# Kernel optimization log

Measured on AMD Instinct MI355X. Metric: run time of the kernel, lower is better.

The kernel has to match this reference:

```python
import jax, jax.numpy as jnp
import numpy as np

# ---- constants from vecpar / module globals ----
N_SAMPLE = 500000
HID = 64       # shared_layers = [64]
HEAD = 32      # q*_layers width
PERIOD = 30
KAPPA, Y_BAR, B, C = 0.2, 2.0, 1.0, 0.1
GAMMA, RHO, SIGMA, DT = 1.2, 0.03, 0.03, 0.005


def _glorot(key, shape):
    fan_in, fan_out = shape
    std = (2.0 / (fan_in + fan_out)) ** 0.5
    return std * jax.random.normal(key, shape, dtype=jnp.float32)


def setup_inputs() -> dict:
    key = jax.random.key(0)
    ks = jax.random.split(key, 8)
    Y = jax.random.uniform(ks[0], (N_SAMPLE, 2), minval=0.05, maxval=5.0, dtype=jnp.float32)
    z = lambda n: jnp.zeros((n,), dtype=jnp.float32)
    return {
        'Y': Y,
        'W0': _glorot(ks[1], (2, HID)),   'b0': z(HID),
        'Wh1': _glorot(ks[2], (HID, HEAD)), 'bh1': z(HEAD), 'Wo1': _glorot(ks[3], (HEAD, 1)), 'bo1': z(1),
        'Wh2': _glorot(ks[4], (HID, HEAD)), 'bh2': z(HEAD), 'Wo2': _glorot(ks[5], (HEAD, 1)), 'bo2': z(1),
        'Wh3': _glorot(ks[6], (HID, HEAD)), 'bh3': z(HEAD), 'Wo3': _glorot(ks[7], (HEAD, 1)), 'bo3': z(1),
    }


def _net(Y2, Y3, W0, b0, Wh1, bh1, Wo1, bo1, Wh2, bh2, Wo2, bo2, Wh3, bh3, Wo3, bo3):
    # shared trunk: concat -> Dense(64) -> tanh; heads: Dense(32)->tanh->Dense(1)->exp
    h = jnp.tanh(jnp.concatenate([Y2, Y3], axis=1) @ W0 + b0)
    q1 = jnp.exp(jnp.tanh(h @ Wh1 + bh1) @ Wo1 + bo1)
    q2 = jnp.exp(jnp.tanh(h @ Wh2 + bh2) @ Wo2 + bo2)
    q3 = jnp.exp(jnp.tanh(h @ Wh3 + bh3) @ Wo3 + bo3)
    return q1, q2, q3


def _forward(Y, W0, b0, Wh1, bh1, Wo1, bo1, Wh2, bh2, Wo2, bo2, Wh3, bh3, Wo3, bo3):
    params = (W0, b0, Wh1, bh1, Wo1, bo1, Wh2, bh2, Wo2, bo2, Wh3, bh3, Wo3, bo3)
    f = lambda y2, y3: _net(y2, y3, *params)

    def q_and_grads(y2, y3):
        # per-row scalar sensitivities via two jvp passes (equiv. to tape.gradient)
        ones = jnp.ones_like(y2); zeros = jnp.zeros_like(y2)
        (q1, q2, q3), (d12, d22, d32) = jax.jvp(f, (y2, y3), (ones, zeros))
        _, (d13, d23, d33) = jax.jvp(f, (y2, y3), (zeros, ones))
        s11 = d12 * SIGMA / q1; s21 = d22 * SIGMA / q2; s31 = d32 * SIGMA / q3
        s12 = d13 * SIGMA / q1; s22 = d23 * SIGMA / q2; s32 = d33 * SIGMA / q3
        return (q1, q2, q3), (s11, s21, s31, s12, s22, s32)

    n = Y.shape[0]
    Y2 = Y[:, :1]; Y3 = Y[:, 1:2]
    (q1, q2, q3), (s11, s21, s31, s12, s22, s32) = q_and_grads(Y2, Y3)

    # dZ already scaled by sqrt(dt)
    noise = jnp.sqrt(jnp.asarray(DT, Y.dtype)) * jax.random.normal(
        jax.random.key(42), (PERIOD, n, 1, 2), dtype=Y.dtype)

    def step(carry, dZ):
        q1, q2, q3, Y2, Y3, s11, s21, s31, s12, s22, s32, loss = carry
        dZ1 = dZ[..., 0]; dZ2 = dZ[..., 1]
        W = q1 + q2 + q3
        q1h = q1 / W; q2h = q2 / W; q3h = 1 - q1h - q2h
        c = B * q1 - C * q1 ** 2 + Y2 + Y3
        sc1 = B * q1 * s11 - 2 * C * q1 ** 2 * s11 + SIGMA
        sc2 = B * q1 * s12 - 2 * C * q1 ** 2 * s12 + SIGMA
        sW1 = q1 * s11 + q2 * s21 + q3 * s31
        sW2 = q1 * s12 + q2 * s22 + q3 * s32
        g = GAMMA / (GAMMA - 1)
        sJ1 = g * (sc1 / c - sW1 / W); sJ2 = g * (sc2 / c - sW2 / W)
        p1 = (GAMMA * q1h * (s11 ** 2 + s12 ** 2)
              + GAMMA * q2h * (s11 * s21 + s12 * s22)
              + GAMMA * q3h * (s11 * s31 + s12 * s32)
              - (1 - GAMMA) * (sJ1 * s11 + sJ2 * s12))
        p2 = (GAMMA * q1h * (s11 * s21 + s12 * s22)
              + GAMMA * q2h * (s21 ** 2 + s22 ** 2)
              + GAMMA * q3h * (s21 * s31 + s22 * s32)
              - (1 - GAMMA) * (sJ1 * s21 + sJ2 * s22))
        p3 = (GAMMA * q1h * (s11 * s31 + s12 * s32)
              + GAMMA * q2h * (s21 * s31 + s22 * s32)
              + GAMMA * q3h * (s31 ** 2 + s32 ** 2)
              - (1 - GAMMA) * (sJ1 * s31 + sJ2 * s32))
        muY2 = KAPPA * (Y_BAR - Y2); muY3 = KAPPA * (Y_BAR - Y3)
        r = (RHO
             + GAMMA * ((B * q1 - 2 * C * q1 ** 2) * (p1 - (B - C * q1))
                        - C * q1 ** 2 * (s11 ** 2 + s12 ** 2) + muY2 + muY3) / c
             - GAMMA * (GAMMA + 1) / 2 * (sc1 ** 2 + sc2 ** 2) / c ** 2)
        r = r / (1 - GAMMA * (B * q1 - 2 * C * q1 ** 2) / c)
        mu1 = r + p1 - (B - C * q1)
        mu2 = r + p2 - Y2 / q2
        mu3 = r + p3 - Y3 / q3
        q1n = q1 * (1 + mu1 * DT + s11 * dZ1 + s12 * dZ2)
        q2n = q2 * (1 + mu2 * DT + s21 * dZ1 + s22 * dZ2)
        q3n = q3 * (1 + mu3 * DT + s31 * dZ1 + s32 * dZ2)
        Y2n = Y2 + muY2 * DT + SIGMA * dZ1
        Y3n = Y3 + muY3 * DT + SIGMA * dZ2
        (q1t, q2t, q3t), (ns11, ns21, ns31, ns12, ns22, ns32) = q_and_grads(Y2n, Y3n)
        loss = loss + jnp.sum((q1n - q1t) ** 2 + (q2n - q2t) ** 2 + (q3n - q3t) ** 2) / (n * PERIOD)
        return (q1n, q2n, q3n, Y2n, Y3n, ns11, ns21, ns31, ns12, ns22, ns32, loss), None

    init = (q1, q2, q3, Y2, Y3, s11, s21, s31, s12, s22, s32, jnp.asarray(0.0, Y.dtype))
    carry, _ = jax.lax.scan(step, init, noise)
    return carry[-1]


def reference(Y, W0, b0, Wh1, bh1, Wo1, bo1, Wh2, bh2, Wo2, bo2, Wh3, bh3, Wo3, bo3):
    return _forward(Y, W0, b0, Wh1, bh1, Wo1, bo1, Wh2, bh2, Wo2, bo2, Wh3, bh3, Wo3, bo3)
```

## Files before the change

kernel.cpp:

```cpp
#include <hip/hip_runtime.h>
#include <hip/hip_bf16.h>
#include <stdint.h>

#define NB 256
#define PERIOD 30

typedef __bf16  bf16x8 __attribute__((ext_vector_type(8)));
typedef float   f32x4  __attribute__((ext_vector_type(4)));
typedef float   f32x2  __attribute__((ext_vector_type(2)));
typedef unsigned int uint4v __attribute__((ext_vector_type(4)));

__device__ __forceinline__ float frcp(float x){ return __builtin_amdgcn_rcpf(x); }

__device__ __forceinline__ float fast_tanh(float x){
  float e = __expf(2.0f*x);
  return fmaf(-2.0f, frcp(e + 1.0f), 1.0f);
}

__device__ __forceinline__ unsigned int f2bfbits(float x){
  union { __hip_bfloat16 b; unsigned short u; } v;
  v.b = __float2bfloat16(x);
  return (unsigned int)v.u;
}
__device__ __forceinline__ unsigned int pack2bf(float lo, float hi){
  return f2bfbits(lo) | (f2bfbits(hi) << 16);
}

__device__ __forceinline__ void threefry2x32_k42(uint32_t x0, uint32_t x1,
                                                 uint32_t& o0, uint32_t& o1){
  const uint32_t ks0 = 0u, ks1 = 42u, ks2 = 0u ^ 42u ^ 0x1BD11BDAu;
  x0 += ks0; x1 += ks1;
#define TFR(rot) { x0 += x1; x1 = (x1 << (rot)) | (x1 >> (32 - (rot))); x1 ^= x0; }
  TFR(13) TFR(15) TFR(26) TFR(6)
  x0 += ks1; x1 += ks2 + 1u;
  TFR(17) TFR(29) TFR(16) TFR(24)
  x0 += ks2; x1 += ks0 + 2u;
  TFR(13) TFR(15) TFR(26) TFR(6)
  x0 += ks0; x1 += ks1 + 3u;
  TFR(17) TFR(29) TFR(16) TFR(24)
  x0 += ks1; x1 += ks2 + 4u;
  TFR(13) TFR(15) TFR(26) TFR(6)
  x0 += ks2; x1 += ks0 + 5u;
#undef TFR
  o0 = x0; o1 = x1;
}

__device__ __forceinline__ float normal_from_bits(uint32_t bits){
  float f = __uint_as_float((bits >> 9) | 0x3f800000u) - 1.0f;
  const float lo = -0.99999994f;
  float u = fmaf(f, 2.0f, lo);
  u = fmaxf(u, lo);
  float w = -log1pf(-u*u);
  float p;
  if (w < 5.0f){
    float ww = w - 2.5f;
    p = 2.81022636e-08f;
    p = fmaf(p, ww, 3.43273939e-07f);
    p = fmaf(p, ww, -3.5233877e-06f);
    p = fmaf(p, ww, -4.39150654e-06f);
    p = fmaf(p, ww, 0.00021858087f);
    p = fmaf(p, ww, -0.00125372503f);
    p = fmaf(p, ww, -0.00417768164f);
    p = fmaf(p, ww, 0.246640727f);
    p = fmaf(p, ww, 1.50140941f);
  } else {
    float ww = sqrtf(w) - 3.0f;
    p = -0.000200214257f;
    p = fmaf(p, ww, 0.000100950558f);
    p = fmaf(p, ww, 0.00134934322f);
    p = fmaf(p, ww, -0.00367342844f);
    p = fmaf(p, ww, 0.00573950773f);
    p = fmaf(p, ww, -0.0076224613f);
    p = fmaf(p, ww, 0.00943887047f);
    p = fmaf(p, ww, 1.00167406f);
    p = fmaf(p, ww, 2.83297682f);
  }
  return 1.41421356f * (p * u);
}

__device__ __forceinline__ void stage_tile(char* buf, int st, int grp, int colL,
    const unsigned int* hp, const unsigned int* up){
  if (grp == st){
    const int rbase = colL * 128;
    const int sw = (colL & 7) << 4;
#pragma unroll
    for (int w = 0; w < 8; ++w){
      int off = rbase + ((w * 16) ^ sw);
      *(uint4v*)(buf + off)        = uint4v{hp[w*4], hp[w*4+1], hp[w*4+2], hp[w*4+3]};
      *(uint4v*)(buf + 2048 + off) = uint4v{up[w*4], up[w*4+1], up[w*4+2], up[w*4+3]};
    }
  }
}

__device__ __forceinline__ void net_eval(
    float y2, float y3,
    const float* __restrict__ W0, const float* __restrict__ b0,
    char* sAw,
    const char* __restrict__ sBb,
    const float* __restrict__ sBH,
    const float* __restrict__ sWO,
    int colL, int grp,
    const float* bo_v,
    float& q1o, float& q2o, float& q3o,
    float& s11, float& s21, float& s31,
    float& s12, float& s22, float& s32)
{
  unsigned int hp[32], up[32];
#pragma unroll
  for (int d = 0; d < 32; ++d){
    f32x2 w0a = *(const f32x2*)(W0 + 2*d);
    f32x2 w0b = *(const f32x2*)(W0 + 64 + 2*d);
    f32x2 b0v = *(const f32x2*)(b0 + 2*d);
    f32x2 pre = y2 * w0a + (y3 * w0b + b0v);
    float hA = fast_tanh(pre.x), hB = fast_tanh(pre.y);
    f32x2 h  = {hA, hB};
    f32x2 u  = 1.0f - h * h;
    hp[d] = pack2bf(hA, hB);
    up[d] = pack2bf(u.x, u.y);
  }

  float qraw[3] = {0,0,0}, Araw[3] = {0,0,0}, Braw[3] = {0,0,0};
  const int bsw = (colL & 7) << 4;

#pragma unroll 1
  for (int st = 0; st < 4; ++st){
    int zr = 0;
    asm volatile("" : "+v"(zr));

    stage_tile(sAw, st, grp, colL, hp, up);

    bf16x8 afh[2], afu[2];
#pragma unroll
    for (int kt = 0; kt < 2; ++kt){
      int off = colL*128 + ((kt*64 + grp*16) ^ bsw);
      afh[kt] = *(const bf16x8*)(sAw + off);
      afu[kt] = *(const bf16x8*)(sAw + 2048 + off);
    }

#pragma unroll
    for (int hd = 0; hd < 3; ++hd){
      float aq = 0.0f, aA = 0.0f, aB = 0.0f;
#pragma unroll
      for (int nt = 0; nt < 2; ++nt){
        bf16x8 bW[2], bA[2], bB[2];
#pragma unroll
        for (int kt = 0; kt < 2; ++kt){
          int rbase2 = (hd*96 + nt*16 + colL) * 128;
          int ko = ((kt*64 + grp*16) ^ bsw);
          bW[kt] = *(const bf16x8*)(sBb + rbase2 + ko);
          bA[kt] = *(const bf16x8*)(sBb + rbase2 + 4096 + ko);
          bB[kt] = *(const bf16x8*)(sBb + rbase2 + 8192 + ko);
        }
        f32x4 bh4 = *(const f32x4*)(sBH + hd*32 + nt*16 + grp*4 + zr);
        f32x4 wo4 = *(const f32x4*)(sWO + hd*32 + nt*16 + grp*4 + zr);
        f32x4 cAT = bh4;
        f32x4 cA2 = {0,0,0,0}, cA3 = {0,0,0,0};
#pragma unroll
        for (int kt = 0; kt < 2; ++kt){
          cAT = __builtin_amdgcn_mfma_f32_16x16x32_bf16(bW[kt], afh[kt], cAT, 0, 0, 0);
          cA2 = __builtin_amdgcn_mfma_f32_16x16x32_bf16(bA[kt], afu[kt], cA2, 0, 0, 0);
          cA3 = __builtin_amdgcn_mfma_f32_16x16x32_bf16(bB[kt], afu[kt], cA3, 0, 0, 0);
        }
        float t0 = fast_tanh(cAT[0]);
        float t1 = fast_tanh(cAT[1]);
        float t2 = fast_tanh(cAT[2]);
        float t3 = fast_tanh(cAT[3]);
        aq = fmaf(t0, wo4[0], aq);
        aq = fmaf(t1, wo4[1], aq);
        aq = fmaf(t2, wo4[2], aq);
        aq = fmaf(t3, wo4[3], aq);
        float dt0 = fmaf(-t0, t0, 1.0f);
        float dt1 = fmaf(-t1, t1, 1.0f);
        float dt2 = fmaf(-t2, t2, 1.0f);
        float dt3 = fmaf(-t3, t3, 1.0f);
        aA = fmaf(dt0, cA2[0], aA);
        aA = fmaf(dt1, cA2[1], aA);
        aA = fmaf(dt2, cA2[2], aA);
        aA = fmaf(dt3, cA2[3], aA);
        aB = fmaf(dt0, cA3[0], aB);
        aB = fmaf(dt1, cA3[1], aB);
        aB = fmaf(dt2, cA3[2], aB);
        aB = fmaf(dt3, cA3[3], aB);
      }
      aq += __shfl_xor(aq, 16, 64);  aq += __shfl_xor(aq, 32, 64);
      aA += __shfl_xor(aA, 16, 64);  aA += __shfl_xor(aA, 32, 64);
      aB += __shfl_xor(aB, 16, 64);  aB += __shfl_xor(aB, 32, 64);
      bool keep = (st == grp);
      qraw[hd] = keep ? aq : qraw[hd];
      Araw[hd] = keep ? aA : Araw[hd];
      Braw[hd] = keep ? aB : Braw[hd];
    }
  }

  q1o = __expf(qraw[0] + bo_v[0]);
  q2o = __expf(qraw[1] + bo_v[1]);
  q3o = __expf(qraw[2] + bo_v[2]);
  s11 = Araw[0]; s21 = Araw[1]; s31 = Araw[2];
  s12 = Braw[0]; s22 = Braw[1]; s32 = Braw[2];
}

__global__ __launch_bounds__(NB)
void sim_kernel(const float* __restrict__ Y,
  const float* __restrict__ W0,  const float* __restrict__ b0,
  const float* __restrict__ Wh1, const float* __restrict__ bh1,
  const float* __restrict__ Wo1, const float* __restrict__ bo1,
  const float* __restrict__ Wh2, const float* __restrict__ bh2,
  const float* __restrict__ Wo2, const float* __restrict__ bo2,
  const float* __restrict__ Wh3, const float* __restrict__ bh3,
  const float* __restrict__ Wo3, const float* __restrict__ bo3,
  float* __restrict__ out, int n)
{
  __shared__ __align__(16) char sB[288 * 128];
  __shared__ __align__(16) char sA[4][2 * 16 * 128];
  __shared__ __align__(16) float sBH[96];
  __shared__ __align__(16) float sWO[96];

  for (int e = threadIdx.x; e < 18432; e += NB){
    int hd   = e / 6144;
    int rem  = e - hd * 6144;
    int mat  = rem >> 11;
    int rem2 = rem & 2047;
    int j = rem2 >> 5, i = rem2 & 31;
    const float* W  = (hd == 0) ? Wh1 : (hd == 1) ? Wh2 : Wh3;
    const float* WO = (hd == 0) ? Wo1 : (hd == 1) ? Wo2 : Wo3;
    float wh = W[j * 32 + i];
    float sc = WO[i] * 0.03f;
    float v  = (mat == 0) ? wh
             : (mat == 1) ? W0[j] * wh * sc
                          : W0[64 + j] * wh * sc;
    int R   = hd * 96 + mat * 32 + i;
    int off = (R * 128 + j * 2) ^ ((R & 7) << 4);
    *(unsigned short*)(sB + off) = (unsigned short)f2bfbits(v);
  }
  if (threadIdx.x < 96){
    int hd = threadIdx.x >> 5, row = threadIdx.x & 31;
    const float* BH = (hd == 0) ? bh1 : (hd == 1) ? bh2 : bh3;
    const float* WO = (hd == 0) ? Wo1 : (hd == 1) ? Wo2 : Wo3;
    sBH[threadIdx.x] = BH[row];
    sWO[threadIdx.x] = WO[row];
  }
  __syncthreads();

  const int wv   = threadIdx.x >> 6;
  const int lane = threadIdx.x & 63;
  const int colL = lane & 15;
  const int grp  = lane >> 4;
  char* sAw = &sA[wv][0];

  float bo_v[3] = {bo1[0], bo2[0], bo3[0]};

  const int gid = blockIdx.x * NB + threadIdx.x;
  const int ii  = (gid < n) ? gid : (n - 1);
  const float valid = (gid < n) ? 1.0f : 0.0f;

  const float2 yv = ((const float2*)Y)[ii];
  const float y2 = yv.x, y3 = yv.y;

  const float GAMMA = 1.2f, DT = 0.005f, SIGMA = 0.03f;
  const float KAPPA = 0.2f, YBAR = 2.0f, RHO = 0.03f, Bc = 1.0f, Cc = 0.1f;

  float q1,q2,q3,s11,s21,s31,s12,s22,s32;
  net_eval(y2, y3, W0, b0, sAw, sB, sBH, sWO, colL, grp, bo_v,
           q1,q2,q3,s11,s21,s31,s12,s22,s32);
  float Y2 = y2, Y3 = y3;
  float loss = 0.0f;

  for (int t = 0; t < PERIOD; ++t){
    uint32_t idx0 = 2u * ((uint32_t)t * (uint32_t)n + (uint32_t)ii);
    uint32_t a0, a1, c0, c1;
    threefry2x32_k42(0u, idx0,      a0, a1);
    threefry2x32_k42(0u, idx0 + 1u, c0, c1);
    float dZ1 = 0.070710678f * normal_from_bits(a0 ^ a1);
    float dZ2 = 0.070710678f * normal_from_bits(c0 ^ c1);

    float Wt  = q1 + q2 + q3;
    float q1h = q1 / Wt;
    float q2h = q2 / Wt;
    float q3h = 1.0f - q1h - q2h;
    float q1sq = q1 * q1;
    float c   = Bc*q1 - Cc*q1sq + Y2 + Y3;
    float bq  = Bc*q1 - 2.0f*Cc*q1sq;
    float sc1 = fmaf(bq, s11, SIGMA);
    float sc2 = fmaf(bq, s12, SIGMA);
    float sW1 = q1*s11 + q2*s21 + q3*s31;
    float sW2 = q1*s12 + q2*s22 + q3*s32;
    float sJ1 = 6.0f * (sc1/c - sW1/Wt);
    float sJ2 = 6.0f * (sc2/c - sW2/Wt);
    float d11 = s11*s11 + s12*s12;
    float d12 = s11*s21 + s12*s22;
    float d13 = s11*s31 + s12*s32;
    float d22 = s21*s21 + s22*s22;
    float d23 = s21*s31 + s22*s32;
    float d33 = s31*s31 + s32*s32;
    const float oneMG = 1.0f - GAMMA;
    float p1 = GAMMA*(q1h*d11 + q2h*d12 + q3h*d13) - oneMG*(sJ1*s11 + sJ2*s12);
    float p2 = GAMMA*(q1h*d12 + q2h*d22 + q3h*d23) - oneMG*(sJ1*s21 + sJ2*s22);
    float p3 = GAMMA*(q1h*d13 + q2h*d23 + q3h*d33) - oneMG*(sJ1*s31 + sJ2*s32);
    float muY2 = KAPPA * (YBAR - Y2);
    float muY3 = KAPPA * (YBAR - Y3);
    float r = RHO + GAMMA*(bq*(p1 - (Bc - Cc*q1)) - Cc*q1sq*d11 + muY2 + muY3)/c
                  - 1.32f*(sc1*sc1 + sc2*sc2)/(c*c);
    r = r / (1.0f - GAMMA*bq/c);
    float mu1 = r + p1 - (Bc - Cc*q1);
    float mu2 = r + p2 - Y2/q2;
    float mu3 = r + p3 - Y3/q3;
    float q1n = q1 * (1.0f + mu1*DT + s11*dZ1 + s12*dZ2);
    float q2n = q2 * (1.0f + mu2*DT + s21*dZ1 + s22*dZ2);
    float q3n = q3 * (1.0f + mu3*DT + s31*dZ1 + s32*dZ2);
    float Y2n = Y2 + muY2*DT + SIGMA*dZ1;
    float Y3n = Y3 + muY3*DT + SIGMA*dZ2;

    float qt1, qt2, qt3;
    net_eval(Y2n, Y3n, W0, b0, sAw, sB, sBH, sWO, colL, grp, bo_v,
             qt1,qt2,qt3, s11,s21,s31,s12,s22,s32);

    float e1 = q1n - qt1, e2 = q2n - qt2, e3 = q3n - qt3;
    loss += e1*e1 + e2*e2 + e3*e3;

    q1 = q1n; q2 = q2n; q3 = q3n; Y2 = Y2n; Y3 = Y3n;
  }

  loss *= valid * (1.0f / ((float)15000000));

#pragma unroll
  for (int off = 32; off > 0; off >>= 1)
    loss += __shfl_down(loss, off, 64);
  __shared__ float sred[NB / 64];
  if (lane == 0) sred[wv] = loss;
  __syncthreads();
  if (threadIdx.x == 0){
    float s = 0.0f;
#pragma unroll
    for (int w = 0; w < NB / 64; ++w) s += sred[w];
    atomicAdd(out, s);
  }
}

extern "C" void kernel_launch(void* const* d_in, const int* in_sizes, int n_in,
                              void* d_out, int out_size, void* d_ws, size_t ws_size,
                              hipStream_t stream)
{
  const float* Y   = (const float*)d_in[0];
  const float* W0  = (const float*)d_in[1];
  const float* b0  = (const float*)d_in[2];
  const float* Wh1 = (const float*)d_in[3];
  const float* bh1 = (const float*)d_in[4];
  const float* Wo1 = (const float*)d_in[5];
  const float* bo1 = (const float*)d_in[6];
  const float* Wh2 = (const float*)d_in[7];
  const float* bh2 = (const float*)d_in[8];
  const float* Wo2 = (const float*)d_in[9];
  const float* bo2 = (const float*)d_in[10];
  const float* Wh3 = (const float*)d_in[11];
  const float* bh3 = (const float*)d_in[12];
  const float* Wo3 = (const float*)d_in[13];
  const float* bo3 = (const float*)d_in[14];

  const int n = in_sizes[0] / 2;

  (void)hipMemsetAsync(d_out, 0, sizeof(float), stream);

  const int grid = (n + NB - 1) / NB;
  sim_kernel<<<grid, NB, 0, stream>>>(Y,
      W0, b0, Wh1, bh1, Wo1, bo1, Wh2, bh2, Wo2, bo2, Wh3, bh3, Wo3, bo3,
      (float*)d_out, n);
}
```

Baseline: 2.478 ms.

## Process two samples per thread so MFMA weight fragments are reused

Each thread now handles two sample rows, and the network evaluation runs eight 16-row tiles per wave instead of four. Each B-weight fragment load from LDS is amortised over more MFMA work, and the grid is halved. The hidden bias is now added after the MFMA rather than used as the accumulator init, and the bias/output-weight loads are hoisted out of the inner loop. The cost is roughly doubled register pressure (two hp/up arrays of 32 words each) and fewer blocks, which may lower occupancy or cause spills.

```diff
diff --git a/kernel.cpp b/kernel.cpp
--- a/kernel.cpp
+++ b/kernel.cpp
@@ -78,9 +78,9 @@
   return 1.41421356f * (p * u);
 }
 
-__device__ __forceinline__ void stage_tile(char* buf, int st, int grp, int colL,
+__device__ __forceinline__ void stage_tile(char* buf, int tile, int grp, int colL,
     const unsigned int* hp, const unsigned int* up){
-  if (grp == st){
+  if (grp == tile){
     const int rbase = colL * 128;
     const int sw = (colL & 7) << 4;
 #pragma unroll
@@ -92,42 +92,92 @@
   }
 }
 
-__device__ __forceinline__ void net_eval(
-    float y2, float y3,
+__device__ __forceinline__ void step_math(
+    float dZ1, float dZ2,
+    float q1, float q2, float q3, float Y2, float Y3,
+    float s11, float s21, float s31, float s12, float s22, float s32,
+    float& q1n, float& q2n, float& q3n, float& Y2n, float& Y3n)
+{
+  const float GAMMA = 1.2f, DT = 0.005f, SIGMA = 0.03f;
+  const float KAPPA = 0.2f, YBAR = 2.0f, RHO = 0.03f, Bc = 1.0f, Cc = 0.1f;
+  float Wt  = q1 + q2 + q3;
+  float q1h = q1 / Wt;
+  float q2h = q2 / Wt;
+  float q3h = 1.0f - q1h - q2h;
+  float q1sq = q1 * q1;
+  float c   = Bc*q1 - Cc*q1sq + Y2 + Y3;
+  float bq  = Bc*q1 - 2.0f*Cc*q1sq;
+  float sc1 = fmaf(bq, s11, SIGMA);
+  float sc2 = fmaf(bq, s12, SIGMA);
+  float sW1 = q1*s11 + q2*s21 + q3*s31;
+  float sW2 = q1*s12 + q2*s22 + q3*s32;
+  float sJ1 = 6.0f * (sc1/c - sW1/Wt);
+  float sJ2 = 6.0f * (sc2/c - sW2/Wt);
+  float d11 = s11*s11 + s12*s12;
+  float d12 = s11*s21 + s12*s22;
+  float d13 = s11*s31 + s12*s32;
+  float d22 = s21*s21 + s22*s22;
+  float d23 = s21*s31 + s22*s32;
+  float d33 = s31*s31 + s32*s32;
+  const float oneMG = 1.0f - GAMMA;
+  float p1 = GAMMA*(q1h*d11 + q2h*d12 + q3h*d13) - oneMG*(sJ1*s11 + sJ2*s12);
+  float p2 = GAMMA*(q1h*d12 + q2h*d22 + q3h*d23) - oneMG*(sJ1*s21 + sJ2*s22);
+  float p3 = GAMMA*(q1h*d13 + q2h*d23 + q3h*d33) - oneMG*(sJ1*s31 + sJ2*s32);
+  float muY2 = KAPPA * (YBAR - Y2);
+  float muY3 = KAPPA * (YBAR - Y3);
+  float r = RHO + GAMMA*(bq*(p1 - (Bc - Cc*q1)) - Cc*q1sq*d11 + muY2 + muY3)/c
+                - 1.32f*(sc1*sc1 + sc2*sc2)/(c*c);
+  r = r / (1.0f - GAMMA*bq/c);
+  float mu1 = r + p1 - (Bc - Cc*q1);
+  float mu2 = r + p2 - Y2/q2;
+  float mu3 = r + p3 - Y3/q3;
+  q1n = q1 * (1.0f + mu1*DT + s11*dZ1 + s12*dZ2);
+  q2n = q2 * (1.0f + mu2*DT + s21*dZ1 + s22*dZ2);
+  q3n = q3 * (1.0f + mu3*DT + s31*dZ1 + s32*dZ2);
+  Y2n = Y2 + muY2*DT + SIGMA*dZ1;
+  Y3n = Y3 + muY3*DT + SIGMA*dZ2;
+}
+
+__device__ __forceinline__ void net_eval2(
+    float y2a, float y3a, float y2b, float y3b,
     const float* __restrict__ W0, const float* __restrict__ b0,
-    char* sAw,
-    const char* __restrict__ sBb,
-    const float* __restrict__ sBH,
-    const float* __restrict__ sWO,
-    int colL, int grp,
-    const float* bo_v,
-    float& q1o, float& q2o, float& q3o,
-    float& s11, float& s21, float& s31,
-    float& s12, float& s22, float& s32)
+    char* sAw, const char* __restrict__ sBb,
+    const float* __restrict__ sBH, const float* __restrict__ sWO,
+    int colL, int grp, const float* bo_v,
+    float& q1a, float& q2a, float& q3a,
+    float& s11a, float& s21a, float& s31a,
+    float& s12a, float& s22a, float& s32a,
+    float& q1b, float& q2b, float& q3b,
+    float& s11b, float& s21b, float& s31b,
+    float& s12b, float& s22b, float& s32b)
 {
-  unsigned int hp[32], up[32];
+  unsigned int hp0[32], up0[32], hp1[32], up1[32];
 #pragma unroll
   for (int d = 0; d < 32; ++d){
     f32x2 w0a = *(const f32x2*)(W0 + 2*d);
     f32x2 w0b = *(const f32x2*)(W0 + 64 + 2*d);
     f32x2 b0v = *(const f32x2*)(b0 + 2*d);
-    f32x2 pre = y2 * w0a + (y3 * w0b + b0v);
-    float hA = fast_tanh(pre.x), hB = fast_tanh(pre.y);
-    f32x2 h  = {hA, hB};
-    f32x2 u  = 1.0f - h * h;
-    hp[d] = pack2bf(hA, hB);
-    up[d] = pack2bf(u.x, u.y);
-  }
-
-  float qraw[3] = {0,0,0}, Araw[3] = {0,0,0}, Braw[3] = {0,0,0};
+    f32x2 preA = y2a * w0a + (y3a * w0b + b0v);
+    f32x2 preB = y2b * w0a + (y3b * w0b + b0v);
+    float a0 = fast_tanh(preA.x), a1 = fast_tanh(preA.y);
+    float b0_ = fast_tanh(preB.x), b1 = fast_tanh(preB.y);
+    hp0[d] = pack2bf(a0, a1);
+    up0[d] = pack2bf(fmaf(-a0, a0, 1.0f), fmaf(-a1, a1, 1.0f));
+    hp1[d] = pack2bf(b0_, b1);
+    up1[d] = pack2bf(fmaf(-b0_, b0_, 1.0f), fmaf(-b1, b1, 1.0f));
+  }
+
+  float qr0[3] = {0,0,0}, Ar0[3] = {0,0,0}, Br0[3] = {0,0,0};
+  float qr1[3] = {0,0,0}, Ar1[3] = {0,0,0}, Br1[3] = {0,0,0};
   const int bsw = (colL & 7) << 4;
 
 #pragma unroll 1
-  for (int st = 0; st < 4; ++st){
+  for (int st = 0; st < 8; ++st){
     int zr = 0;
     asm volatile("" : "+v"(zr));
 
-    stage_tile(sAw, st, grp, colL, hp, up);
+    if (st < 4) stage_tile(sAw, st,     grp, colL, hp0, up0);
+    else        stage_tile(sAw, st - 4, grp, colL, hp1, up1);
 
     bf16x8 afh[2], afu[2];
 #pragma unroll
@@ -139,6 +189,10 @@
 
 #pragma unroll
     for (int hd = 0; hd < 3; ++hd){
+      f32x4 bh4_0 = *(const f32x4*)(sBH + hd*32 +      grp*4 + zr);
+      f32x4 wo4_0 = *(const f32x4*)(sWO + hd*32 +      grp*4 + zr);
+      f32x4 bh4_1 = *(const f32x4*)(sBH + hd*32 + 16 + grp*4 + zr);
+      f32x4 wo4_1 = *(const f32x4*)(sWO + hd*32 + 16 + grp*4 + zr);
       float aq = 0.0f, aA = 0.0f, aB = 0.0f;
 #pragma unroll
       for (int nt = 0; nt < 2; ++nt){
@@ -151,20 +205,19 @@
           bA[kt] = *(const bf16x8*)(sBb + rbase2 + 4096 + ko);
           bB[kt] = *(const bf16x8*)(sBb + rbase2 + 8192 + ko);
         }
-        f32x4 bh4 = *(const f32x4*)(sBH + hd*32 + nt*16 + grp*4 + zr);
-        f32x4 wo4 = *(const f32x4*)(sWO + hd*32 + nt*16 + grp*4 + zr);
-        f32x4 cAT = bh4;
-        f32x4 cA2 = {0,0,0,0}, cA3 = {0,0,0,0};
+        f32x4 cAT = {0,0,0,0}, cA2 = {0,0,0,0}, cA3 = {0,0,0,0};
 #pragma unroll
         for (int kt = 0; kt < 2; ++kt){
           cAT = __builtin_amdgcn_mfma_f32_16x16x32_bf16(bW[kt], afh[kt], cAT, 0, 0, 0);
           cA2 = __builtin_amdgcn_mfma_f32_16x16x32_bf16(bA[kt], afu[kt], cA2, 0, 0, 0);
           cA3 = __builtin_amdgcn_mfma_f32_16x16x32_bf16(bB[kt], afu[kt], cA3, 0, 0, 0);
         }
-        float t0 = fast_tanh(cAT[0]);
-        float t1 = fast_tanh(cAT[1]);
-        float t2 = fast_tanh(cAT[2]);
-        float t3 = fast_tanh(cAT[3]);
+        f32x4 bh4 = nt ? bh4_1 : bh4_0;
+        f32x4 wo4 = nt ? wo4_1 : wo4_0;
+        float t0 = fast_tanh(cAT[0] + bh4[0]);
+        float t1 = fast_tanh(cAT[1] + bh4[1]);
+        float t2 = fast_tanh(cAT[2] + bh4[2]);
+        float t3 = fast_tanh(cAT[3] + bh4[3]);
         aq = fmaf(t0, wo4[0], aq);
         aq = fmaf(t1, wo4[1], aq);
         aq = fmaf(t2, wo4[2], aq);
@@ -185,18 +238,24 @@
       aq += __shfl_xor(aq, 16, 64);  aq += __shfl_xor(aq, 32, 64);
       aA += __shfl_xor(aA, 16, 64);  aA += __shfl_xor(aA, 32, 64);
       aB += __shfl_xor(aB, 16, 64);  aB += __shfl_xor(aB, 32, 64);
-      bool keep = (st == grp);
-      qraw[hd] = keep ? aq : qraw[hd];
-      Araw[hd] = keep ? aA : Araw[hd];
-      Braw[hd] = keep ? aB : Braw[hd];
+      bool k0 = (st == grp);
+      bool k1 = (st == grp + 4);
+      qr0[hd] = k0 ? aq : qr0[hd];  qr1[hd] = k1 ? aq : qr1[hd];
+      Ar0[hd] = k0 ? aA : Ar0[hd];  Ar1[hd] = k1 ? aA : Ar1[hd];
+      Br0[hd] = k0 ? aB : Br0[hd];  Br1[hd] = k1 ? aB : Br1[hd];
     }
   }
 
-  q1o = __expf(qraw[0] + bo_v[0]);
-  q2o = __expf(qraw[1] + bo_v[1]);
-  q3o = __expf(qraw[2] + bo_v[2]);
-  s11 = Araw[0]; s21 = Araw[1]; s31 = Araw[2];
-  s12 = Braw[0]; s22 = Braw[1]; s32 = Braw[2];
+  q1a = __expf(qr0[0] + bo_v[0]);
+  q2a = __expf(qr0[1] + bo_v[1]);
+  q3a = __expf(qr0[2] + bo_v[2]);
+  s11a = Ar0[0]; s21a = Ar0[1]; s31a = Ar0[2];
+  s12a = Br0[0]; s22a = Br0[1]; s32a = Br0[2];
+  q1b = __expf(qr1[0] + bo_v[0]);
+  q2b = __expf(qr1[1] + bo_v[1]);
+  q3b = __expf(qr1[2] + bo_v[2]);
+  s11b = Ar1[0]; s21b = Ar1[1]; s31b = Ar1[2];
+  s12b = Br1[0]; s22b = Br1[1]; s32b = Br1[2];
 }
 
 __global__ __launch_bounds__(NB)
@@ -249,78 +308,63 @@
 
   float bo_v[3] = {bo1[0], bo2[0], bo3[0]};
 
-  const int gid = blockIdx.x * NB + threadIdx.x;
-  const int ii  = (gid < n) ? gid : (n - 1);
-  const float valid = (gid < n) ? 1.0f : 0.0f;
-
-  const float2 yv = ((const float2*)Y)[ii];
-  const float y2 = yv.x, y3 = yv.y;
-
-  const float GAMMA = 1.2f, DT = 0.005f, SIGMA = 0.03f;
-  const float KAPPA = 0.2f, YBAR = 2.0f, RHO = 0.03f, Bc = 1.0f, Cc = 0.1f;
-
-  float q1,q2,q3,s11,s21,s31,s12,s22,s32;
-  net_eval(y2, y3, W0, b0, sAw, sB, sBH, sWO, colL, grp, bo_v,
-           q1,q2,q3,s11,s21,s31,s12,s22,s32);
-  float Y2 = y2, Y3 = y3;
-  float loss = 0.0f;
+  const int base = blockIdx.x * (2 * NB) + wv * 128;
+  const int iiA  = base + lane;
+  const int iiB  = base + 64 + lane;
+  const int iA   = (iiA < n) ? iiA : (n - 1);
+  const int iB   = (iiB < n) ? iiB : (n - 1);
+  const float validA = (iiA < n) ? 1.0f : 0.0f;
+  const float validB = (iiB < n) ? 1.0f : 0.0f;
+
+  const float2 yvA = ((const float2*)Y)[iA];
+  const float2 yvB = ((const float2*)Y)[iB];
+
+  float q1a,q2a,q3a,s11a,s21a,s31a,s12a,s22a,s32a;
+  float q1b,q2b,q3b,s11b,s21b,s31b,s12b,s22b,s32b;
+  net_eval2(yvA.x, yvA.y, yvB.x, yvB.y, W0, b0, sAw, sB, sBH, sWO,
+            colL, grp, bo_v,
+            q1a,q2a,q3a,s11a,s21a,s31a,s12a,s22a,s32a,
+            q1b,q2b,q3b,s11b,s21b,s31b,s12b,s22b,s32b);
+  float Y2a = yvA.x, Y3a = yvA.y;
+  float Y2b = yvB.x, Y3b = yvB.y;
+  float lossA = 0.0f, lossB = 0.0f;
 
   for (int t = 0; t < PERIOD; ++t){
-    uint32_t idx0 = 2u * ((uint32_t)t * (uint32_t)n + (uint32_t)ii);
-    uint32_t a0, a1, c0, c1;
-    threefry2x32_k42(0u, idx0,      a0, a1);
-    threefry2x32_k42(0u, idx0 + 1u, c0, c1);
-    float dZ1 = 0.070710678f * normal_from_bits(a0 ^ a1);
-    float dZ2 = 0.070710678f * normal_from_bits(c0 ^ c1);
-
-    float Wt  = q1 + q2 + q3;
-    float q1h = q1 / Wt;
-    float q2h = q2 / Wt;
-    float q3h = 1.0f - q1h - q2h;
-    float q1sq = q1 * q1;
-    float c   = Bc*q1 - Cc*q1sq + Y2 + Y3;
-    float bq  = Bc*q1 - 2.0f*Cc*q1sq;
-    float sc1 = fmaf(bq, s11, SIGMA);
-    float sc2 = fmaf(bq, s12, SIGMA);
-    float sW1 = q1*s11 + q2*s21 + q3*s31;
-    float sW2 = q1*s12 + q2*s22 + q3*s32;
-    float sJ1 = 6.0f * (sc1/c - sW1/Wt);
-    float sJ2 = 6.0f * (sc2/c - sW2/Wt);
-    float d11 = s11*s11 + s12*s12;
-    float d12 = s11*s21 + s12*s22;
-    float d13 = s11*s31 + s12*s32;
-    float d22 = s21*s21 + s22*s22;
-    float d23 = s21*s31 + s22*s32;
-    float d33 = s31*s31 + s32*s32;
-    const float oneMG = 1.0f - GAMMA;
-    float p1 = GAMMA*(q1h*d11 + q2h*d12 + q3h*d13) - oneMG*(sJ1*s11 + sJ2*s12);
-    float p2 = GAMMA*(q1h*d12 + q2h*d22 + q3h*d23) - oneMG*(sJ1*s21 + sJ2*s22);
-    float p3 = GAMMA*(q1h*d13 + q2h*d23 + q3h*d33) - oneMG*(sJ1*s31 + sJ2*s32);
-    float muY2 = KAPPA * (YBAR - Y2);
-    float muY3 = KAPPA * (YBAR - Y3);
-    float r = RHO + GAMMA*(bq*(p1 - (Bc - Cc*q1)) - Cc*q1sq*d11 + muY2 + muY3)/c
-                  - 1.32f*(sc1*sc1 + sc2*sc2)/(c*c);
-    r = r / (1.0f - GAMMA*bq/c);
-    float mu1 = r + p1 - (Bc - Cc*q1);
-    float mu2 = r + p2 - Y2/q2;
-    float mu3 = r + p3 - Y3/q3;
-    float q1n = q1 * (1.0f + mu1*DT + s11*dZ1 + s12*dZ2);
-    float q2n = q2 * (1.0f + mu2*DT + s21*dZ1 + s22*dZ2);
-    float q3n = q3 * (1.0f + mu3*DT + s31*dZ1 + s32*dZ2);
-    float Y2n = Y2 + muY2*DT + SIGMA*dZ1;
-    float Y3n = Y3 + muY3*DT + SIGMA*dZ2;
-
-    float qt1, qt2, qt3;
-    net_eval(Y2n, Y3n, W0, b0, sAw, sB, sBH, sWO, colL, grp, bo_v,
-             qt1,qt2,qt3, s11,s21,s31,s12,s22,s32);
-
-    float e1 = q1n - qt1, e2 = q2n - qt2, e3 = q3n - qt3;
-    loss += e1*e1 + e2*e2 + e3*e3;
-
-    q1 = q1n; q2 = q2n; q3 = q3n; Y2 = Y2n; Y3 = Y3n;
-  }
-
-  loss *= valid * (1.0f / ((float)15000000));
+    uint32_t iA0 = 2u * ((uint32_t)t * (uint32_t)n + (uint32_t)iA);
+    uint32_t iB0 = 2u * ((uint32_t)t * (uint32_t)n + (uint32_t)iB);
+    uint32_t a0,a1,c0,c1,e0,e1,g0,g1;
+    threefry2x32_k42(0u, iA0,      a0, a1);
+    threefry2x32_k42(0u, iA0 + 1u, c0, c1);
+    threefry2x32_k42(0u, iB0,      e0, e1);
+    threefry2x32_k42(0u, iB0 + 1u, g0, g1);
+    float dZ1a = 0.070710678f * normal_from_bits(a0 ^ a1);
+    float dZ2a = 0.070710678f * normal_from_bits(c0 ^ c1);
+    float dZ1b = 0.070710678f * normal_from_bits(e0 ^ e1);
+    float dZ2b = 0.070710678f * normal_from_bits(g0 ^ g1);
+
+    float q1na,q2na,q3na,Y2na,Y3na;
+    float q1nb,q2nb,q3nb,Y2nb,Y3nb;
+    step_math(dZ1a, dZ2a, q1a,q2a,q3a,Y2a,Y3a,
+              s11a,s21a,s31a,s12a,s22a,s32a, q1na,q2na,q3na,Y2na,Y3na);
+    step_math(dZ1b, dZ2b, q1b,q2b,q3b,Y2b,Y3b,
+              s11b,s21b,s31b,s12b,s22b,s32b, q1nb,q2nb,q3nb,Y2nb,Y3nb);
+
+    float qt1a,qt2a,qt3a, qt1b,qt2b,qt3b;
+    net_eval2(Y2na, Y3na, Y2nb, Y3nb, W0, b0, sAw, sB, sBH, sWO,
+              colL, grp, bo_v,
+              qt1a,qt2a,qt3a, s11a,s21a,s31a,s12a,s22a,s32a,
+              qt1b,qt2b,qt3b, s11b,s21b,s31b,s12b,s22b,s32b);
+
+    float e1a = q1na - qt1a, e2a = q2na - qt2a, e3a = q3na - qt3a;
+    float e1b = q1nb - qt1b, e2b = q2nb - qt2b, e3b = q3nb - qt3b;
+    lossA += e1a*e1a + e2a*e2a + e3a*e3a;
+    lossB += e1b*e1b + e2b*e2b + e3b*e3b;
+
+    q1a = q1na; q2a = q2na; q3a = q3na; Y2a = Y2na; Y3a = Y3na;
+    q1b = q1nb; q2b = q2nb; q3b = q3nb; Y2b = Y2nb; Y3b = Y3nb;
+  }
+
+  float loss = (lossA * validA + lossB * validB) * (1.0f / ((float)15000000));
 
 #pragma unroll
   for (int off = 32; off > 0; off >>= 1)
@@ -360,7 +404,7 @@
 
   (void)hipMemsetAsync(d_out, 0, sizeof(float), stream);
 
-  const int grid = (n + NB - 1) / NB;
+  const int grid = (n + 2*NB - 1) / (2*NB);
   sim_kernel<<<grid, NB, 0, stream>>>(Y,
       W0, b0, Wh1, bh1, Wo1, bo1, Wh2, bh2, Wo2, bo2, Wh3, bh3, Wo3, bo3,
       (float*)d_out, n);
```

New measurement: 2.587 ms. 1.04x slower.
